# Performance work log

Hardware: AMD Instinct MI355X
Metric: run time of the kernel (lower is better)

## Reference

```python
import jax, jax.numpy as jnp
import numpy as np

D_H = 768
HEAD = 12
D_ATTN = D_H // HEAD


def setup_inputs() -> dict:
    key = jax.random.key(0)
    ks = jax.random.split(key, 9)
    bz, slen = 2, 4096
    scale = 1.0 / np.sqrt(D_H)
    return {
        "v": jax.random.normal(ks[0], (bz, slen, D_H), jnp.float32),
        "k": jax.random.normal(ks[1], (bz, slen, D_H), jnp.float32),
        "q": jax.random.normal(ks[2], (bz, slen, D_H), jnp.float32),
        "mask": jax.random.randint(ks[3], (bz, 1, 1, slen), 0, 2, jnp.int32),
        "w_v": jax.random.normal(ks[4], (D_H, D_H), jnp.float32) * scale,
        "w_k": jax.random.normal(ks[5], (D_H, D_H), jnp.float32) * scale,
        "w_q": jax.random.normal(ks[6], (D_H, D_H), jnp.float32) * scale,
        "w_o": jax.random.normal(ks[7], (D_H, D_H), jnp.float32) * scale,
        "b_o": jax.random.normal(ks[8], (D_H,), jnp.float32) * 0.02,
    }


def _split_head(x, seq_len):
    # (bz, len, d_h) -> (bz, head, len, d_attn)
    bz = x.shape[0]
    return x.reshape(bz, seq_len, HEAD, D_ATTN).transpose(0, 2, 1, 3)


def reference(v, k, q, mask, w_v, w_k, w_q, w_o, b_o):
    len_k, len_q = k.shape[1], q.shape[1]
    vh = _split_head(v @ w_v, len_k)   # (bz, head, len_k, d_attn)
    kh = _split_head(k @ w_k, len_k)
    qh = _split_head(q @ w_q, len_q)
    # scaled dot-product attention with additive mask
    weight = jnp.einsum("bhqd,bhkd->bhqk", qh, kh) / jnp.sqrt(
        jnp.asarray(D_ATTN, jnp.float32)
    )
    weight = weight + mask.astype(weight.dtype) * (-1e9)
    scale_weight = jax.nn.softmax(weight, axis=-1)
    attn = jnp.einsum("bhqk,bhkd->bhqd", scale_weight, vh)
    attn = attn.transpose(0, 2, 1, 3).reshape(-1, len_q, D_H)
    return attn @ w_o + b_o
```

## Files before the change

### kernel.cpp

```cpp
#include <hip/hip_runtime.h>
#include <hip/hip_bf16.h>

#define SLEN 4096
#define DH 768
#define NHEAD 12
#define DA 64

using short8 = __attribute__((ext_vector_type(8))) short;
using f32x4  = __attribute__((ext_vector_type(4))) float;
typedef unsigned uv2 __attribute__((ext_vector_type(2)));

static __device__ __forceinline__ unsigned short f2b(float f) {
    union { __hip_bfloat16 h; unsigned short u; } c;
    c.h = __float2bfloat16(f);
    return c.u;
}

static __device__ __forceinline__ unsigned pkbf(float a, float b) {
    __hip_bfloat162 h = __float22bfloat162_rn(float2{a, b});
    union { __hip_bfloat162 h; unsigned u; } c; c.h = h; return c.u;
}

static __device__ __forceinline__ float fexp2(float x) {
    float r; asm("v_exp_f32 %0, %1" : "=v"(r) : "v"(x)); return r;
}

static __device__ __forceinline__ void swap32(unsigned& a, unsigned& b, int g1) {
#if __has_builtin(__builtin_amdgcn_permlane32_swap)
    uv2 r = __builtin_amdgcn_permlane32_swap(a, b, false, false);
    a = r.x; b = r.y;
#else
    unsigned own = g1 ? b : a, send = g1 ? a : b;
    unsigned recv = __shfl_xor(send, 32);
    unsigned nlo = g1 ? recv : own;
    unsigned nhi = g1 ? own : recv;
    a = nlo; b = nhi;
#endif
}

static __device__ __forceinline__ void swap16(unsigned& a, unsigned& b, int g0) {
#if __has_builtin(__builtin_amdgcn_permlane16_swap)
    uv2 r = __builtin_amdgcn_permlane16_swap(a, b, false, false);
    a = r.x; b = r.y;
#else
    unsigned own = g0 ? b : a, send = g0 ? a : b;
    unsigned recv = __shfl_xor(send, 16);
    unsigned nlo = g0 ? recv : own;
    unsigned nhi = g0 ? own : recv;
    a = nlo; b = nhi;
#endif
}

#define GLD_LDS16(gp, lp) __builtin_amdgcn_global_load_lds( \
    (const __attribute__((address_space(1))) unsigned int*)(gp), \
    (__attribute__((address_space(3))) unsigned int*)(lp), 16, 0, 0)

#define CSCALE 0.18033688011f
#define BIASSTRIDE 4352

__global__ __launch_bounds__(256) void wtrans4(const float* __restrict__ w_v, const float* __restrict__ w_k,
                                               const float* __restrict__ w_q, const float* __restrict__ w_o,
                                               unsigned short* __restrict__ WtV, unsigned short* __restrict__ WtK,
                                               unsigned short* __restrict__ WtQ, unsigned short* __restrict__ WtO,
                                               const int* __restrict__ mask, int* __restrict__ idx,
                                               float* __restrict__ biasC, int* __restrict__ nktArr) {
    const int z = blockIdx.y;
    const int t = threadIdx.x;
    if (z == 4) {
        if (blockIdx.x >= 2) return;
        __shared__ int psum[256];
        const int b = blockIdx.x;
        const int s0 = t * 16;
        const int* mb = mask + b * SLEN;
        int keep[16]; int cnt = 0;
#pragma unroll
        for (int j = 0; j < 16; ++j) { keep[j] = (mb[s0 + j] == 0); cnt += keep[j]; }
        psum[t] = cnt;
        __syncthreads();
        for (int off = 1; off < 256; off <<= 1) {
            int v = psum[t];
            int u = (t >= off) ? psum[t - off] : 0;
            __syncthreads();
            psum[t] = v + u;
            __syncthreads();
        }
        int excl = psum[t] - cnt;
        int total = psum[255];
        int* ib = idx + b * SLEN;
#pragma unroll
        for (int j = 0; j < 16; ++j)
            if (keep[j]) ib[excl++] = s0 + j;
        for (int j = total + t; j < SLEN; j += 256) ib[j] = 0;
        int nkt = (total + 63) >> 6;
        if (nkt < 2) nkt = 2;
        if (t == 0) nktArr[b] = nkt;
        float* bb = biasC + b * BIASSTRIDE;
        for (int j = t; j < BIASSTRIDE; j += 256) bb[j] = (j < total) ? 0.f : -1.442695041e9f;
        return;
    }
    const float* W = (z == 0) ? w_v : (z == 1) ? w_k : (z == 2) ? w_q : w_o;
    unsigned short* Wt = (z == 0) ? WtV : (z == 1) ? WtK : (z == 2) ? WtQ : WtO;
    __shared__ float tile[64][65];
    const int tk = blockIdx.x / 12, tn = blockIdx.x % 12;
    const int k0 = tk * 64, n0 = tn * 64;
#pragma unroll
    for (int i = 0; i < 4; ++i) {
        int uid = t + 256 * i;
        int r = uid >> 4, c = (uid & 15) * 4;
        float4 v4 = *reinterpret_cast<const float4*>(W + (size_t)(k0 + r) * DH + n0 + c);
        tile[r][c] = v4.x; tile[r][c + 1] = v4.y; tile[r][c + 2] = v4.z; tile[r][c + 3] = v4.w;
    }
    __syncthreads();
#pragma unroll
    for (int i = 0; i < 2; ++i) {
        int uid = t + 256 * i;
        int n = uid >> 3, c = (uid & 7) * 8;
        union { unsigned short us[8]; uint4 u; } pk;
#pragma unroll
        for (int j = 0; j < 8; ++j) pk.us[j] = f2b(tile[c + j][n]);
        *reinterpret_cast<uint4*>(Wt + (size_t)(n0 + n) * DH + k0 + c) = pk.u;
    }
}

__global__ __launch_bounds__(256, 3) void proj3(const float* __restrict__ vin, const float* __restrict__ kin,
                                                const float* __restrict__ qin,
                                                const unsigned short* __restrict__ WtV,
                                                const unsigned short* __restrict__ WtK,
                                                const unsigned short* __restrict__ WtQ,
                                                unsigned short* __restrict__ Vh,
                                                unsigned short* __restrict__ Kh,
                                                unsigned short* __restrict__ Qh) {
    __shared__ __align__(16) char smem[49152];
    const int t = threadIdx.x;
    const int w = t >> 6, lane = t & 63, lr = lane & 15, lg = lane >> 4;
    const int zz = blockIdx.y;
    const int z = zz / 6, panel = zz % 6;
    const float* X = (z == 0) ? vin : (z == 1) ? kin : qin;
    const unsigned short* Wt = (z == 0) ? WtV : (z == 1) ? WtK : WtQ;
    const int row0 = blockIdx.x * 128;
    const int n0 = panel * 128;

    const float* ap[4];
#pragma unroll
    for (int g = 0; g < 4; ++g) {
        int row = w * 32 + g * 8 + (lane >> 3);
        int cj = (lane & 7) ^ (row & 7);
        ap[g] = X + (size_t)(row0 + row) * DH + cj * 4;
    }
    const unsigned short* bp2[2];
#pragma unroll
    for (int g = 0; g < 2; ++g) {
        int n = w * 32 + g * 16 + (lane >> 2);
        int cj = (lane & 3) ^ (n & 3);
        bp2[g] = Wt + (size_t)(n0 + n) * DH + cj * 8;
    }

    const int arow = w * 32 + lr;
    const int lr7 = lr & 7, lr3 = lr & 3;

    f32x4 acc[2][8] = {};

#define STAGE(PAR) do {                                                              \
        char* ab_ = smem + (PAR) * 16384 + w * 4096;                                 \
        char* bb_ = smem + 32768 + (PAR) * 8192 + w * 2048;                          \
        GLD_LDS16(ap[0], ab_);         GLD_LDS16(ap[1], ab_ + 1024);                 \
        GLD_LDS16(ap[2], ab_ + 2048);  GLD_LDS16(ap[3], ab_ + 3072);                 \
        GLD_LDS16(bp2[0], bb_);        GLD_LDS16(bp2[1], bb_ + 1024);                \
        ap[0] += 32; ap[1] += 32; ap[2] += 32; ap[3] += 32;                          \
        bp2[0] += 32; bp2[1] += 32;                                                  \
    } while (0)

    STAGE(0);
    __syncthreads();

    for (int kt = 0; kt < 24; ++kt) {
        const int par = kt & 1;
        if (kt < 23) STAGE(par ^ 1);
        const char* bufA = smem + par * 16384;
        const char* bufB = smem + 32768 + par * 8192;
        short8 af[2];
#pragma unroll
        for (int mi = 0; mi < 2; ++mi) {
            int r = arow + mi * 16;
            f32x4 alo = *reinterpret_cast<const f32x4*>(bufA + r * 128 + ((2 * lg) ^ lr7) * 16);
            f32x4 ahi = *reinterpret_cast<const f32x4*>(bufA + r * 128 + ((2 * lg + 1) ^ lr7) * 16);
            union { unsigned u[4]; short8 s; } pk;
            pk.u[0] = pkbf(alo[0], alo[1]);
            pk.u[1] = pkbf(alo[2], alo[3]);
            pk.u[2] = pkbf(ahi[0], ahi[1]);
            pk.u[3] = pkbf(ahi[2], ahi[3]);
            af[mi] = pk.s;
        }
        __builtin_amdgcn_s_setprio(1);
#pragma unroll
        for (int ni = 0; ni < 8; ++ni) {
            int n = ni * 16 + lr;
            short8 bf = *reinterpret_cast<const short8*>(bufB + n * 64 + (lg ^ lr3) * 16);
            acc[0][ni] = __builtin_amdgcn_mfma_f32_16x16x32_bf16(af[0], bf, acc[0][ni], 0, 0, 0);
            acc[1][ni] = __builtin_amdgcn_mfma_f32_16x16x32_bf16(af[1], bf, acc[1][ni], 0, 0, 0);
        }
        __builtin_amdgcn_s_setprio(0);
        __syncthreads();
    }
#undef STAGE

    const int b = row0 >> 12, s0 = row0 & 4095;
    unsigned short* Y = (z == 0) ? Vh : (z == 1) ? Kh : Qh;
    const float scale = (z == 2) ? CSCALE : 1.0f;
#pragma unroll
    for (int mi = 0; mi < 2; ++mi)
#pragma unroll
        for (int ni = 0; ni < 8; ++ni) {
            int n = n0 + ni * 16 + lr;
            int h = n >> 6, d = n & 63;
#pragma unroll
            for (int r = 0; r < 4; ++r) {
                int s = s0 + w * 32 + mi * 16 + lg * 4 + r;
                Y[(size_t)((b * NHEAD + h) * SLEN + s) * DA + d] = f2b(acc[mi][ni][r] * scale);
            }
        }
}

__global__ __launch_bounds__(256) void kvcompact(const unsigned short* __restrict__ Kh,
                                                 const unsigned short* __restrict__ Vh,
                                                 unsigned short* __restrict__ Khc,
                                                 unsigned short* __restrict__ VhTc,
                                                 const int* __restrict__ idx,
                                                 const int* __restrict__ nktArr) {
    const int jt = blockIdx.x;
    const int bh = blockIdx.y;
    const int b = bh / NHEAD;
    if (jt >= nktArr[b]) return;
    const int j0 = jt * 64;
    __shared__ unsigned short tile[64][72];
    const int t = threadIdx.x;
    const int r = t >> 2, c = t & 3;
    const int src = idx[b * SLEN + j0 + r];
    const size_t kin  = ((size_t)bh * SLEN + src) * DA + c * 16;
    const size_t kout = ((size_t)bh * SLEN + j0 + r) * DA + c * 16;
    uint4 kv0 = *reinterpret_cast<const uint4*>(Kh + kin);
    uint4 kv1 = *reinterpret_cast<const uint4*>(Kh + kin + 8);
    *reinterpret_cast<uint4*>(Khc + kout) = kv0;
    *reinterpret_cast<uint4*>(Khc + kout + 8) = kv1;
    uint4 vv0 = *reinterpret_cast<const uint4*>(Vh + kin);
    uint4 vv1 = *reinterpret_cast<const uint4*>(Vh + kin + 8);
    *reinterpret_cast<uint4*>(&tile[r][c * 16]) = vv0;
    *reinterpret_cast<uint4*>(&tile[r][c * 16 + 8]) = vv1;
    __syncthreads();
    const int d = t & 63, jc = (t >> 6) * 16;
    union { unsigned short us[8]; uint4 u; } p0, p1;
#pragma unroll
    for (int j = 0; j < 8; ++j) { p0.us[j] = tile[jc + j][d]; p1.us[j] = tile[jc + 8 + j][d]; }
    unsigned short* dst = VhTc + ((size_t)bh * DA + d) * SLEN + j0 + jc;
    *reinterpret_cast<uint4*>(dst) = p0.u;
    *reinterpret_cast<uint4*>(dst + 8) = p1.u;
}

__global__ __launch_bounds__(256, 3) void attn_kernel(const unsigned short* __restrict__ Qh,
                                                      const unsigned short* __restrict__ Kh,
                                                      const unsigned short* __restrict__ VhT,
                                                      const float* __restrict__ biasC,
                                                      const int* __restrict__ nktArr,
                                                      unsigned short* __restrict__ AT) {
    __shared__ __align__(16) char smem[49152];
    const int t = threadIdx.x;
    const int w = t >> 6, lane = t & 63, lr = lane & 15, lg = lane >> 4;
    const int g0 = (lane >> 4) & 1, g1 = (lane >> 5) & 1;
    const int lr7 = lr & 7;

    const int i = blockIdx.x;
    const int bh = (i & 7) * 3 + ((i >> 3) >> 5);
    const int qb = (i >> 3) & 31;
    const int b = bh / NHEAD;
    const int q0 = qb * 128;
    const size_t base = (size_t)bh * SLEN * DA;
    const int wq0 = q0 + w * 32;
    const int nkt = nktArr[b];

    short8 qf[2][2];
#pragma unroll
    for (int mi = 0; mi < 2; ++mi)
#pragma unroll
        for (int ks = 0; ks < 2; ++ks)
            qf[mi][ks] = *reinterpret_cast<const short8*>(
                Qh + base + (size_t)(wq0 + mi * 16 + lr) * DA + ks * 32 + lg * 8);

    const int uid0 = (w << 6) | lane;
    const int r0 = uid0 >> 3;
    const int sc0 = ((uid0 & 7) ^ (r0 & 7)) * 8;
    const unsigned short* kp = Kh + base + (size_t)r0 * DA + sc0;
    const unsigned short* vp = VhT + ((size_t)bh * DA + r0) * SLEN + sc0;
    const float* bp = biasC + b * BIASSTRIDE + lg * 4;

    const int a0 = lr * 128 + ((lg) ^ lr7) * 16;
    const int a1 = lr * 128 + ((4 + lg) ^ lr7) * 16;

    f32x4 st[2][4];
    f32x4 oacc[2][4] = {};
    f32x4 oacc_l[2] = {};
    f32x4 bias_c[4];
    short8 pa[2][2];
    union { unsigned u[4]; short8 s; } ones;
    ones.u[0] = 0x3F803F80u; ones.u[1] = 0x3F803F80u; ones.u[2] = 0x3F803F80u; ones.u[3] = 0x3F803F80u;

#define STAGE(CB) do {                                                   \
        GLD_LDS16(kp,              smem + (CB) + w * 1024);              \
        GLD_LDS16(kp + 2048,       smem + (CB) + (4 + w) * 1024);        \
        GLD_LDS16(vp,              smem + (CB) + 8192 + w * 1024);       \
        GLD_LDS16(vp + 32 * SLEN,  smem + (CB) + 8192 + (4 + w) * 1024); \
        kp += 64 * DA; vp += 64;                                         \
    } while (0)

#define BIASLD do {                                                              \
        _Pragma("unroll") for (int ni = 0; ni < 4; ++ni)                         \
            bias_c[ni] = *reinterpret_cast<const f32x4*>(bp + ni * 16);          \
        bp += 64;                                                                \
    } while (0)

#define QKT(NB) do {                                                                           \
        _Pragma("unroll") for (int ni = 0; ni < 4; ++ni) {                                     \
            short8 kf0 = *reinterpret_cast<const short8*>(smem + (NB) + ni * 2048 + a0);       \
            short8 kf1 = *reinterpret_cast<const short8*>(smem + (NB) + ni * 2048 + a1);       \
            st[0][ni] = __builtin_amdgcn_mfma_f32_16x16x32_bf16(kf1, qf[0][1],                 \
                        __builtin_amdgcn_mfma_f32_16x16x32_bf16(kf0, qf[0][0], bias_c[ni], 0, 0, 0), 0, 0, 0); \
            st[1][ni] = __builtin_amdgcn_mfma_f32_16x16x32_bf16(kf1, qf[1][1],                 \
                        __builtin_amdgcn_mfma_f32_16x16x32_bf16(kf0, qf[1][0], bias_c[ni], 0, 0, 0), 0, 0, 0); \
        }                                                                                      \
    } while (0)

#define PV(CB) do {                                                                                  \
        _Pragma("unroll") for (int ni = 0; ni < 4; ++ni) {                                           \
            short8 vf0 = *reinterpret_cast<const short8*>(smem + (CB) + 8192 + ni * 2048 + a0);      \
            short8 vf1 = *reinterpret_cast<const short8*>(smem + (CB) + 8192 + ni * 2048 + a1);      \
            oacc[0][ni] = __builtin_amdgcn_mfma_f32_16x16x32_bf16(vf0, pa[0][0], oacc[0][ni], 0, 0, 0); \
            oacc[0][ni] = __builtin_amdgcn_mfma_f32_16x16x32_bf16(vf1, pa[0][1], oacc[0][ni], 0, 0, 0); \
            oacc[1][ni] = __builtin_amdgcn_mfma_f32_16x16x32_bf16(vf0, pa[1][0], oacc[1][ni], 0, 0, 0); \
            oacc[1][ni] = __builtin_amdgcn_mfma_f32_16x16x32_bf16(vf1, pa[1][1], oacc[1][ni], 0, 0, 0); \
        }                                                                                            \
        oacc_l[0] = __builtin_amdgcn_mfma_f32_16x16x32_bf16(ones.s, pa[0][0], oacc_l[0], 0, 0, 0);   \
        oacc_l[0] = __builtin_amdgcn_mfma_f32_16x16x32_bf16(ones.s, pa[0][1], oacc_l[0], 0, 0, 0);   \
        oacc_l[1] = __builtin_amdgcn_mfma_f32_16x16x32_bf16(ones.s, pa[1][0], oacc_l[1], 0, 0, 0);   \
        oacc_l[1] = __builtin_amdgcn_mfma_f32_16x16x32_bf16(ones.s, pa[1][1], oacc_l[1], 0, 0, 0);   \
    } while (0)

#define SOFTMAX do {                                                                               \
        _Pragma("unroll") for (int mi = 0; mi < 2; ++mi) {                                         \
            unsigned D[8];                                                                         \
            _Pragma("unroll") for (int ni = 0; ni < 4; ++ni) {                                     \
                float p0 = fexp2(st[mi][ni][0]);                                                   \
                float p1 = fexp2(st[mi][ni][1]);                                                   \
                float p2 = fexp2(st[mi][ni][2]);                                                   \
                float p3 = fexp2(st[mi][ni][3]);                                                   \
                D[ni * 2] = pkbf(p0, p1);                                                          \
                D[ni * 2 + 1] = pkbf(p2, p3);                                                      \
            }                                                                                      \
            swap32(D[0], D[2], g1); swap32(D[1], D[3], g1);                                        \
            swap32(D[4], D[6], g1); swap32(D[5], D[7], g1);                                        \
            swap16(D[0], D[2], g0); swap16(D[1], D[3], g0);                                        \
            swap16(D[4], D[6], g0); swap16(D[4 - 4], D[2], g0);                                    \
            union { unsigned u[4]; short8 s; } c0, c1;                                             \
            c0.u[0] = D[0]; c0.u[1] = D[1]; c0.u[2] = D[2]; c0.u[3] = D[3];                        \
            c1.u[0] = D[4]; c1.u[1] = D[5]; c1.u[2] = D[6]; c1.u[3] = D[7];                        \
            pa[mi][0] = c0.s; pa[mi][1] = c1.s;                                                    \
        }                                                                                          \
    } while (0)

#undef SOFTMAX
#define SOFTMAX do {                                                                               \
        _Pragma("unroll") for (int mi = 0; mi < 2; ++mi) {                                         \
            unsigned D[8];                                                                         \
            _Pragma("unroll") for (int ni = 0; ni < 4; ++ni) {                                     \
                float p0 = fexp2(st[mi][ni][0]);                                                   \
                float p1 = fexp2(st[mi][ni][1]);                                                   \
                float p2 = fexp2(st[mi][ni][2]);                                                   \
                float p3 = fexp2(st[mi][ni][3]);                                                   \
                D[ni * 2] = pkbf(p0, p1);                                                          \
                D[ni * 2 + 1] = pkbf(p2, p3);                                                      \
            }                                                                                      \
            swap32(D[0], D[2], g1); swap32(D[1], D[3], g1);                                        \
            swap32(D[4], D[6], g1); swap32(D[5], D[7], g1);                                        \
            swap16(D[0], D[2], g0); swap16(D[1], D[3], g0);                                        \
            swap16(D[4], D[6], g0); swap16(D[5], D[7], g0);                                        \
            union { unsigned u[4]; short8 s; } c0, c1;                                             \
            c0.u[0] = D[0]; c0.u[1] = D[1]; c0.u[2] = D[2]; c0.u[3] = D[3];                        \
            c1.u[0] = D[4]; c1.u[1] = D[5]; c1.u[2] = D[6]; c1.u[3] = D[7];                        \
            pa[mi][0] = c0.s; pa[mi][1] = c1.s;                                                    \
        }                                                                                          \
    } while (0)

    STAGE(0);
    __syncthreads();
    STAGE(16384);
    BIASLD;
    __builtin_amdgcn_s_setprio(1);
    QKT(0);
    __builtin_amdgcn_s_setprio(0);

    int cb = 0, nb = 16384, nnb = 32768;
    for (int kt = 0; kt < nkt - 1; ++kt) {
        SOFTMAX;
        __syncthreads();
        if (kt < nkt - 2) STAGE(nnb);
        BIASLD;
        __builtin_amdgcn_s_setprio(1);
        QKT(nb);
        PV(cb);
        __builtin_amdgcn_s_setprio(0);
        int tmp = cb; cb = nb; nb = nnb; nnb = tmp;
    }
    SOFTMAX;
    __builtin_amdgcn_s_setprio(1);
    PV(cb);
    __builtin_amdgcn_s_setprio(0);

#undef SOFTMAX
#undef PV
#undef QKT
#undef BIASLD
#undef STAGE

    {
        __syncthreads();
        float inv[2];
        inv[0] = 1.0f / oacc_l[0][0];
        inv[1] = 1.0f / oacc_l[1][0];
        unsigned* Obw = reinterpret_cast<unsigned*>(smem) + w * (32 * 36);
#pragma unroll
        for (int mi = 0; mi < 2; ++mi)
#pragma unroll
            for (int ni = 0; ni < 4; ++ni) {
                uint2 pr;
                pr.x = pkbf(oacc[mi][ni][0] * inv[mi], oacc[mi][ni][1] * inv[mi]);
                pr.y = pkbf(oacc[mi][ni][2] * inv[mi], oacc[mi][ni][3] * inv[mi]);
                *reinterpret_cast<uint2*>(&Obw[(mi * 16 + lr) * 36 + ni * 8 + lg * 2]) = pr;
            }
        __syncthreads();
        int row = lane >> 1, half = lane & 1;
        int qg = q0 + w * 32 + row;
        unsigned short* dst = AT + (size_t)(b * SLEN + qg) * DH + (bh % NHEAD) * DA + half * 32;
#pragma unroll
        for (int c = 0; c < 4; ++c) {
            uint4 v = *reinterpret_cast<const uint4*>(&Obw[row * 36 + half * 16 + c * 4]);
            *reinterpret_cast<uint4*>(dst + c * 8) = v;
        }
    }
}

__global__ __launch_bounds__(256, 3) void proj_out(const unsigned short* __restrict__ X,
                                                   const unsigned short* __restrict__ Wt,
                                                   const float* __restrict__ bias,
                                                   float* __restrict__ Y) {
    __shared__ __align__(16) char smem[49152];
    const int t = threadIdx.x;
    const int w = t >> 6, lane = t & 63, lr = lane & 15, lg = lane >> 4;
    const int row0 = blockIdx.x * 128;
    const int n0 = blockIdx.y * 64;
    const int lr7 = lr & 7;

    const unsigned short* ap[4];
#pragma unroll
    for (int g = 0; g < 4; ++g) {
        int row = w * 32 + g * 8 + (lane >> 3);
        int cj = (lane & 7) ^ (row & 7);
        ap[g] = X + (size_t)(row0 + row) * DH + cj * 8;
    }
    const unsigned short* bp2[2];
#pragma unroll
    for (int g = 0; g < 2; ++g) {
        int n = w * 16 + g * 8 + (lane >> 3);
        int cj = (lane & 7) ^ (n & 7);
        bp2[g] = Wt + (size_t)(n0 + n) * DH + cj * 8;
    }

    f32x4 acc[2][4] = {};

#define STAGE_O(PAR) do {                                                            \
        char* ab_ = smem + (PAR) * 16384 + w * 4096;                                 \
        char* bb_ = smem + 32768 + (PAR) * 8192 + w * 2048;                          \
        GLD_LDS16(ap[0], ab_);         GLD_LDS16(ap[1], ab_ + 1024);                 \
        GLD_LDS16(ap[2], ab_ + 2048);  GLD_LDS16(ap[3], ab_ + 3072);                 \
        GLD_LDS16(bp2[0], bb_);        GLD_LDS16(bp2[1], bb_ + 1024);                \
        ap[0] += 64; ap[1] += 64; ap[2] += 64; ap[3] += 64;                          \
        bp2[0] += 64; bp2[1] += 64;                                                  \
    } while (0)

    STAGE_O(0);
    __syncthreads();

    for (int kt = 0; kt < 12; ++kt) {
        const int par = kt & 1;
        if (kt < 11) STAGE_O(par ^ 1);
        const char* bufA = smem + par * 16384;
        const char* bufB = smem + 32768 + par * 8192;
        short8 af[2][2], bf[4][2];
#pragma unroll
        for (int mi = 0; mi < 2; ++mi) {
            int r = w * 32 + mi * 16 + lr;
#pragma unroll
            for (int ks = 0; ks < 2; ++ks)
                af[mi][ks] = *reinterpret_cast<const short8*>(bufA + r * 128 + ((ks * 4 + lg) ^ lr7) * 16);
        }
#pragma unroll
        for (int ni = 0; ni < 4; ++ni) {
            int n = ni * 16 + lr;
#pragma unroll
            for (int ks = 0; ks < 2; ++ks)
                bf[ni][ks] = *reinterpret_cast<const short8*>(bufB + n * 128 + ((ks * 4 + lg) ^ lr7) * 16);
        }
        __builtin_amdgcn_s_setprio(1);
#pragma unroll
        for (int mi = 0; mi < 2; ++mi)
#pragma unroll
            for (int ni = 0; ni < 4; ++ni) {
                acc[mi][ni] = __builtin_amdgcn_mfma_f32_16x16x32_bf16(af[mi][0], bf[ni][0], acc[mi][ni], 0, 0, 0);
                acc[mi][ni] = __builtin_amdgcn_mfma_f32_16x16x32_bf16(af[mi][1], bf[ni][1], acc[mi][ni], 0, 0, 0);
            }
        __builtin_amdgcn_s_setprio(0);
        __syncthreads();
    }
#undef STAGE_O

#pragma unroll
    for (int ni = 0; ni < 4; ++ni) {
        float bv = bias[n0 + ni * 16 + lr];
#pragma unroll
        for (int mi = 0; mi < 2; ++mi)
#pragma unroll
            for (int r = 0; r < 4; ++r) {
                int row = row0 + w * 32 + mi * 16 + lg * 4 + r;
                Y[(size_t)row * DH + n0 + ni * 16 + lr] = acc[mi][ni][r] + bv;
            }
    }
}

extern "C" void kernel_launch(void* const* d_in, const int* in_sizes, int n_in,
                              void* d_out, int out_size, void* d_ws, size_t ws_size,
                              hipStream_t stream) {
    const float* v   = (const float*)d_in[0];
    const float* k   = (const float*)d_in[1];
    const float* q   = (const float*)d_in[2];
    const int*  mask = (const int*)d_in[3];
    const float* w_v = (const float*)d_in[4];
    const float* w_k = (const float*)d_in[5];
    const float* w_q = (const float*)d_in[6];
    const float* w_o = (const float*)d_in[7];
    const float* b_o = (const float*)d_in[8];
    float* out = (float*)d_out;

    char* ws = (char*)d_ws;
    unsigned short* Qh  = (unsigned short*)(ws);
    unsigned short* KhD = (unsigned short*)(ws + 12582912);
    unsigned short* VhD = (unsigned short*)(ws + 25165824);
    unsigned short* Khc = (unsigned short*)(ws + 37748736);
    unsigned short* VhTc= (unsigned short*)(ws + 50331648);
    unsigned short* AT  = KhD;
    unsigned short* WtV = (unsigned short*)(ws + 62914560);
    unsigned short* WtK = WtV + 589824;
    unsigned short* WtQ = WtK + 589824;
    unsigned short* WtO = WtQ + 589824;
    float* biasC = (float*)(ws + 67633152);
    int*   idxA  = (int*)(ws + 67667968);
    int*   nktA  = (int*)(ws + 67700736);

    wtrans4<<<dim3(144, 5), 256, 0, stream>>>(w_v, w_k, w_q, w_o, WtV, WtK, WtQ, WtO,
                                              mask, idxA, biasC, nktA);
    proj3<<<dim3(64, 18), 256, 0, stream>>>(v, k, q, WtV, WtK, WtQ, VhD, KhD, Qh);
    kvcompact<<<dim3(64, 24), 256, 0, stream>>>(KhD, VhD, Khc, VhTc, idxA, nktA);
    attn_kernel<<<768, 256, 0, stream>>>(Qh, Khc, VhTc, biasC, nktA, AT);
    proj_out<<<dim3(64, 12), 256, 0, stream>>>(AT, WtO, b_o, out);
}
```

Baseline: 147.0 us.

## Load V fragments directly from global memory into registers, halving LDS staging

V tiles are no longer staged through LDS. Each lane now loads its V^T MFMA fragments straight from global memory into registers just before the PV step, and only K is triple-buffered in shared memory, so LDS use drops from 48KB to 24KB. This removes the LDS traffic for V and may allow more resident blocks per CU. In exchange, V loads are no longer prefetched a stage ahead, so their global latency sits right before PV and may stall it. Register pressure also rises under the 3-waves launch bound. A dead duplicate softmax macro is also deleted.

```diff
diff --git a/kernel.cpp b/kernel.cpp
--- a/kernel.cpp
+++ b/kernel.cpp
@@ -262,7 +262,7 @@
                                                       const float* __restrict__ biasC,
                                                       const int* __restrict__ nktArr,
                                                       unsigned short* __restrict__ AT) {
-    __shared__ __align__(16) char smem[49152];
+    __shared__ __align__(16) char smem[24576];
     const int t = threadIdx.x;
     const int w = t >> 6, lane = t & 63, lr = lane & 15, lg = lane >> 4;
     const int g0 = (lane >> 4) & 1, g1 = (lane >> 5) & 1;
@@ -289,8 +289,11 @@
     const int r0 = uid0 >> 3;
     const int sc0 = ((uid0 & 7) ^ (r0 & 7)) * 8;
     const unsigned short* kp = Kh + base + (size_t)r0 * DA + sc0;
-    const unsigned short* vp = VhT + ((size_t)bh * DA + r0) * SLEN + sc0;
     const float* bp = biasC + b * BIASSTRIDE + lg * 4;
+    const unsigned short* vq[4];
+#pragma unroll
+    for (int ni = 0; ni < 4; ++ni)
+        vq[ni] = VhT + ((size_t)bh * DA + ni * 16 + lr) * SLEN + lg * 8;
 
     const int a0 = lr * 128 + ((lg) ^ lr7) * 16;
     const int a1 = lr * 128 + ((4 + lg) ^ lr7) * 16;
@@ -300,21 +303,28 @@
     f32x4 oacc_l[2] = {};
     f32x4 bias_c[4];
     short8 pa[2][2];
+    short8 vf[4][2];
     union { unsigned u[4]; short8 s; } ones;
     ones.u[0] = 0x3F803F80u; ones.u[1] = 0x3F803F80u; ones.u[2] = 0x3F803F80u; ones.u[3] = 0x3F803F80u;
 
 #define STAGE(CB) do {                                                   \
-        GLD_LDS16(kp,              smem + (CB) + w * 1024);              \
-        GLD_LDS16(kp + 2048,       smem + (CB) + (4 + w) * 1024);        \
-        GLD_LDS16(vp,              smem + (CB) + 8192 + w * 1024);       \
-        GLD_LDS16(vp + 32 * SLEN,  smem + (CB) + 8192 + (4 + w) * 1024); \
-        kp += 64 * DA; vp += 64;                                         \
+        GLD_LDS16(kp,        smem + (CB) + w * 1024);                    \
+        GLD_LDS16(kp + 2048, smem + (CB) + (4 + w) * 1024);              \
+        kp += 64 * DA;                                                   \
     } while (0)
 
 #define BIASLD do {                                                              \
         _Pragma("unroll") for (int ni = 0; ni < 4; ++ni)                         \
             bias_c[ni] = *reinterpret_cast<const f32x4*>(bp + ni * 16);          \
         bp += 64;                                                                \
+    } while (0)
+
+#define VFLOAD do {                                                              \
+        _Pragma("unroll") for (int ni = 0; ni < 4; ++ni) {                       \
+            vf[ni][0] = *reinterpret_cast<const short8*>(vq[ni]);                \
+            vf[ni][1] = *reinterpret_cast<const short8*>(vq[ni] + 32);           \
+            vq[ni] += 64;                                                        \
+        }                                                                        \
     } while (0)
 
 #define QKT(NB) do {                                                                           \
@@ -328,14 +338,12 @@
         }                                                                                      \
     } while (0)
 
-#define PV(CB) do {                                                                                  \
+#define PV do {                                                                                      \
         _Pragma("unroll") for (int ni = 0; ni < 4; ++ni) {                                           \
-            short8 vf0 = *reinterpret_cast<const short8*>(smem + (CB) + 8192 + ni * 2048 + a0);      \
-            short8 vf1 = *reinterpret_cast<const short8*>(smem + (CB) + 8192 + ni * 2048 + a1);      \
-            oacc[0][ni] = __builtin_amdgcn_mfma_f32_16x16x32_bf16(vf0, pa[0][0], oacc[0][ni], 0, 0, 0); \
-            oacc[0][ni] = __builtin_amdgcn_mfma_f32_16x16x32_bf16(vf1, pa[0][1], oacc[0][ni], 0, 0, 0); \
-            oacc[1][ni] = __builtin_amdgcn_mfma_f32_16x16x32_bf16(vf0, pa[1][0], oacc[1][ni], 0, 0, 0); \
-            oacc[1][ni] = __builtin_amdgcn_mfma_f32_16x16x32_bf16(vf1, pa[1][1], oacc[1][ni], 0, 0, 0); \
+            oacc[0][ni] = __builtin_amdgcn_mfma_f32_16x16x32_bf16(vf[ni][0], pa[0][0], oacc[0][ni], 0, 0, 0); \
+            oacc[0][ni] = __builtin_amdgcn_mfma_f32_16x16x32_bf16(vf[ni][1], pa[0][1], oacc[0][ni], 0, 0, 0); \
+            oacc[1][ni] = __builtin_amdgcn_mfma_f32_16x16x32_bf16(vf[ni][0], pa[1][0], oacc[1][ni], 0, 0, 0); \
+            oacc[1][ni] = __builtin_amdgcn_mfma_f32_16x16x32_bf16(vf[ni][1], pa[1][1], oacc[1][ni], 0, 0, 0); \
         }                                                                                            \
         oacc_l[0] = __builtin_amdgcn_mfma_f32_16x16x32_bf16(ones.s, pa[0][0], oacc_l[0], 0, 0, 0);   \
         oacc_l[0] = __builtin_amdgcn_mfma_f32_16x16x32_bf16(ones.s, pa[0][1], oacc_l[0], 0, 0, 0);   \
@@ -343,29 +351,6 @@
         oacc_l[1] = __builtin_amdgcn_mfma_f32_16x16x32_bf16(ones.s, pa[1][1], oacc_l[1], 0, 0, 0);   \
     } while (0)
 
-#define SOFTMAX do {                                                                               \
-        _Pragma("unroll") for (int mi = 0; mi < 2; ++mi) {                                         \
-            unsigned D[8];                                                                         \
-            _Pragma("unroll") for (int ni = 0; ni < 4; ++ni) {                                     \
-                float p0 = fexp2(st[mi][ni][0]);                                                   \
-                float p1 = fexp2(st[mi][ni][1]);                                                   \
-                float p2 = fexp2(st[mi][ni][2]);                                                   \
-                float p3 = fexp2(st[mi][ni][3]);                                                   \
-                D[ni * 2] = pkbf(p0, p1);                                                          \
-                D[ni * 2 + 1] = pkbf(p2, p3);                                                      \
-            }                                                                                      \
-            swap32(D[0], D[2], g1); swap32(D[1], D[3], g1);                                        \
-            swap32(D[4], D[6], g1); swap32(D[5], D[7], g1);                                        \
-            swap16(D[0], D[2], g0); swap16(D[1], D[3], g0);                                        \
-            swap16(D[4], D[6], g0); swap16(D[4 - 4], D[2], g0);                                    \
-            union { unsigned u[4]; short8 s; } c0, c1;                                             \
-            c0.u[0] = D[0]; c0.u[1] = D[1]; c0.u[2] = D[2]; c0.u[3] = D[3];                        \
-            c1.u[0] = D[4]; c1.u[1] = D[5]; c1.u[2] = D[6]; c1.u[3] = D[7];                        \
-            pa[mi][0] = c0.s; pa[mi][1] = c1.s;                                                    \
-        }                                                                                          \
-    } while (0)
-
-#undef SOFTMAX
 #define SOFTMAX do {                                                                               \
         _Pragma("unroll") for (int mi = 0; mi < 2; ++mi) {                                         \
             unsigned D[8];                                                                         \
@@ -390,32 +375,35 @@
 
     STAGE(0);
     __syncthreads();
-    STAGE(16384);
+    STAGE(8192);
     BIASLD;
     __builtin_amdgcn_s_setprio(1);
     QKT(0);
     __builtin_amdgcn_s_setprio(0);
 
-    int cb = 0, nb = 16384, nnb = 32768;
+    int cb = 0, nb = 8192, nnb = 16384;
     for (int kt = 0; kt < nkt - 1; ++kt) {
         SOFTMAX;
         __syncthreads();
         if (kt < nkt - 2) STAGE(nnb);
         BIASLD;
+        VFLOAD;
         __builtin_amdgcn_s_setprio(1);
         QKT(nb);
-        PV(cb);
+        PV;
         __builtin_amdgcn_s_setprio(0);
         int tmp = cb; cb = nb; nb = nnb; nnb = tmp;
     }
     SOFTMAX;
+    VFLOAD;
     __builtin_amdgcn_s_setprio(1);
-    PV(cb);
+    PV;
     __builtin_amdgcn_s_setprio(0);
 
 #undef SOFTMAX
 #undef PV
 #undef QKT
+#undef VFLOAD
 #undef BIASLD
 #undef STAGE
 
```

Result: slower. 199.9 us (+36.0%).

## Fuse KV compaction into projection kernel via gathered rows and transposed V store

Applied to the files above, without the earlier changes.

The projection kernel now gathers only the unmasked key/value rows through the compaction index and skips row blocks past the compacted length. K is written directly in compacted form, and V is transposed through shared memory and stored as VhT. This removes the separate kvcompact kernel, its intermediate full-size K/V buffers, and the projection work on masked rows. The cost is indirect row loads in the GEMM A path and an extra LDS transpose epilogue for V.

```diff
diff --git a/kernel.cpp b/kernel.cpp
--- a/kernel.cpp
+++ b/kernel.cpp
@@ -127,9 +127,11 @@
                                                 const unsigned short* __restrict__ WtV,
                                                 const unsigned short* __restrict__ WtK,
                                                 const unsigned short* __restrict__ WtQ,
-                                                unsigned short* __restrict__ Vh,
-                                                unsigned short* __restrict__ Kh,
-                                                unsigned short* __restrict__ Qh) {
+                                                unsigned short* __restrict__ VhTc,
+                                                unsigned short* __restrict__ Khc,
+                                                unsigned short* __restrict__ Qh,
+                                                const int* __restrict__ idx,
+                                                const int* __restrict__ nktArr) {
     __shared__ __align__(16) char smem[49152];
     const int t = threadIdx.x;
     const int w = t >> 6, lane = t & 63, lr = lane & 15, lg = lane >> 4;
@@ -137,15 +139,19 @@
     const int z = zz / 6, panel = zz % 6;
     const float* X = (z == 0) ? vin : (z == 1) ? kin : qin;
     const unsigned short* Wt = (z == 0) ? WtV : (z == 1) ? WtK : WtQ;
-    const int row0 = blockIdx.x * 128;
+    const int b = blockIdx.x >> 5;
+    const int r128 = (blockIdx.x & 31) * 128;
+    const bool gather = (z != 2);
+    if (gather && r128 >= nktArr[b] * 64) return;
     const int n0 = panel * 128;
 
     const float* ap[4];
 #pragma unroll
     for (int g = 0; g < 4; ++g) {
         int row = w * 32 + g * 8 + (lane >> 3);
+        int grow = b * SLEN + (gather ? idx[b * SLEN + r128 + row] : (r128 + row));
         int cj = (lane & 7) ^ (row & 7);
-        ap[g] = X + (size_t)(row0 + row) * DH + cj * 4;
+        ap[g] = X + (size_t)grow * DH + cj * 4;
     }
     const unsigned short* bp2[2];
 #pragma unroll
@@ -204,56 +210,40 @@
     }
 #undef STAGE
 
-    const int b = row0 >> 12, s0 = row0 & 4095;
-    unsigned short* Y = (z == 0) ? Vh : (z == 1) ? Kh : Qh;
-    const float scale = (z == 2) ? CSCALE : 1.0f;
-#pragma unroll
-    for (int mi = 0; mi < 2; ++mi)
-#pragma unroll
-        for (int ni = 0; ni < 8; ++ni) {
-            int n = n0 + ni * 16 + lr;
-            int h = n >> 6, d = n & 63;
-#pragma unroll
-            for (int r = 0; r < 4; ++r) {
-                int s = s0 + w * 32 + mi * 16 + lg * 4 + r;
-                Y[(size_t)((b * NHEAD + h) * SLEN + s) * DA + d] = f2b(acc[mi][ni][r] * scale);
+    if (z == 0) {
+        unsigned short (*tile)[136] = reinterpret_cast<unsigned short(*)[136]>(smem);
+#pragma unroll
+        for (int mi = 0; mi < 2; ++mi)
+#pragma unroll
+            for (int ni = 0; ni < 8; ++ni) {
+                int n = ni * 16 + lr;
+                int j = w * 32 + mi * 16 + lg * 4;
+                *reinterpret_cast<unsigned*>(&tile[n][j])     = pkbf(acc[mi][ni][0], acc[mi][ni][1]);
+                *reinterpret_cast<unsigned*>(&tile[n][j + 2]) = pkbf(acc[mi][ni][2], acc[mi][ni][3]);
             }
-        }
-}
-
-__global__ __launch_bounds__(256) void kvcompact(const unsigned short* __restrict__ Kh,
-                                                 const unsigned short* __restrict__ Vh,
-                                                 unsigned short* __restrict__ Khc,
-                                                 unsigned short* __restrict__ VhTc,
-                                                 const int* __restrict__ idx,
-                                                 const int* __restrict__ nktArr) {
-    const int jt = blockIdx.x;
-    const int bh = blockIdx.y;
-    const int b = bh / NHEAD;
-    if (jt >= nktArr[b]) return;
-    const int j0 = jt * 64;
-    __shared__ unsigned short tile[64][72];
-    const int t = threadIdx.x;
-    const int r = t >> 2, c = t & 3;
-    const int src = idx[b * SLEN + j0 + r];
-    const size_t kin  = ((size_t)bh * SLEN + src) * DA + c * 16;
-    const size_t kout = ((size_t)bh * SLEN + j0 + r) * DA + c * 16;
-    uint4 kv0 = *reinterpret_cast<const uint4*>(Kh + kin);
-    uint4 kv1 = *reinterpret_cast<const uint4*>(Kh + kin + 8);
-    *reinterpret_cast<uint4*>(Khc + kout) = kv0;
-    *reinterpret_cast<uint4*>(Khc + kout + 8) = kv1;
-    uint4 vv0 = *reinterpret_cast<const uint4*>(Vh + kin);
-    uint4 vv1 = *reinterpret_cast<const uint4*>(Vh + kin + 8);
-    *reinterpret_cast<uint4*>(&tile[r][c * 16]) = vv0;
-    *reinterpret_cast<uint4*>(&tile[r][c * 16 + 8]) = vv1;
-    __syncthreads();
-    const int d = t & 63, jc = (t >> 6) * 16;
-    union { unsigned short us[8]; uint4 u; } p0, p1;
-#pragma unroll
-    for (int j = 0; j < 8; ++j) { p0.us[j] = tile[jc + j][d]; p1.us[j] = tile[jc + 8 + j][d]; }
-    unsigned short* dst = VhTc + ((size_t)bh * DA + d) * SLEN + j0 + jc;
-    *reinterpret_cast<uint4*>(dst) = p0.u;
-    *reinterpret_cast<uint4*>(dst + 8) = p1.u;
+        __syncthreads();
+        int n = t >> 1, jc = (t & 1) * 64;
+        unsigned short* dst = VhTc +
+            ((size_t)(b * NHEAD + 2 * panel + (n >> 6)) * DA + (n & 63)) * SLEN + r128 + jc;
+#pragma unroll
+        for (int c = 0; c < 8; ++c)
+            *reinterpret_cast<uint4*>(dst + c * 8) = *reinterpret_cast<const uint4*>(&tile[n][jc + c * 8]);
+    } else {
+        unsigned short* Y = (z == 1) ? Khc : Qh;
+        const float scale = (z == 2) ? CSCALE : 1.0f;
+#pragma unroll
+        for (int mi = 0; mi < 2; ++mi)
+#pragma unroll
+            for (int ni = 0; ni < 8; ++ni) {
+                int n = n0 + ni * 16 + lr;
+                int h = n >> 6, d = n & 63;
+#pragma unroll
+                for (int r = 0; r < 4; ++r) {
+                    int s = r128 + w * 32 + mi * 16 + lg * 4 + r;
+                    Y[(size_t)((b * NHEAD + h) * SLEN + s) * DA + d] = f2b(acc[mi][ni][r] * scale);
+                }
+            }
+    }
 }
 
 __global__ __launch_bounds__(256, 3) void attn_kernel(const unsigned short* __restrict__ Qh,
@@ -343,29 +333,6 @@
         oacc_l[1] = __builtin_amdgcn_mfma_f32_16x16x32_bf16(ones.s, pa[1][1], oacc_l[1], 0, 0, 0);   \
     } while (0)
 
-#define SOFTMAX do {                                                                               \
-        _Pragma("unroll") for (int mi = 0; mi < 2; ++mi) {                                         \
-            unsigned D[8];                                                                         \
-            _Pragma("unroll") for (int ni = 0; ni < 4; ++ni) {                                     \
-                float p0 = fexp2(st[mi][ni][0]);                                                   \
-                float p1 = fexp2(st[mi][ni][1]);                                                   \
-                float p2 = fexp2(st[mi][ni][2]);                                                   \
-                float p3 = fexp2(st[mi][ni][3]);                                                   \
-                D[ni * 2] = pkbf(p0, p1);                                                          \
-                D[ni * 2 + 1] = pkbf(p2, p3);                                                      \
-            }                                                                                      \
-            swap32(D[0], D[2], g1); swap32(D[1], D[3], g1);                                        \
-            swap32(D[4], D[6], g1); swap32(D[5], D[7], g1);                                        \
-            swap16(D[0], D[2], g0); swap16(D[1], D[3], g0);                                        \
-            swap16(D[4], D[6], g0); swap16(D[4 - 4], D[2], g0);                                    \
-            union { unsigned u[4]; short8 s; } c0, c1;                                             \
-            c0.u[0] = D[0]; c0.u[1] = D[1]; c0.u[2] = D[2]; c0.u[3] = D[3];                        \
-            c1.u[0] = D[4]; c1.u[1] = D[5]; c1.u[2] = D[6]; c1.u[3] = D[7];                        \
-            pa[mi][0] = c0.s; pa[mi][1] = c1.s;                                                    \
-        }                                                                                          \
-    } while (0)
-
-#undef SOFTMAX
 #define SOFTMAX do {                                                                               \
         _Pragma("unroll") for (int mi = 0; mi < 2; ++mi) {                                         \
             unsigned D[8];                                                                         \
@@ -548,24 +515,21 @@
     float* out = (float*)d_out;
 
     char* ws = (char*)d_ws;
-    unsigned short* Qh  = (unsigned short*)(ws);
-    unsigned short* KhD = (unsigned short*)(ws + 12582912);
-    unsigned short* VhD = (unsigned short*)(ws + 25165824);
-    unsigned short* Khc = (unsigned short*)(ws + 37748736);
-    unsigned short* VhTc= (unsigned short*)(ws + 50331648);
-    unsigned short* AT  = KhD;
-    unsigned short* WtV = (unsigned short*)(ws + 62914560);
-    unsigned short* WtK = WtV + 589824;
-    unsigned short* WtQ = WtK + 589824;
-    unsigned short* WtO = WtQ + 589824;
-    float* biasC = (float*)(ws + 67633152);
-    int*   idxA  = (int*)(ws + 67667968);
-    int*   nktA  = (int*)(ws + 67700736);
+    unsigned short* Qh   = (unsigned short*)(ws);
+    unsigned short* Khc  = (unsigned short*)(ws + 12582912);
+    unsigned short* AT   = (unsigned short*)(ws + 25165824);
+    unsigned short* VhTc = (unsigned short*)(ws + 37748736);
+    unsigned short* WtV  = (unsigned short*)(ws + 50331648);
+    unsigned short* WtK  = WtV + 589824;
+    unsigned short* WtQ  = WtK + 589824;
+    unsigned short* WtO  = WtQ + 589824;
+    float* biasC = (float*)(ws + 55050240);
+    int*   idxA  = (int*)(ws + 55085056);
+    int*   nktA  = (int*)(ws + 55117824);
 
     wtrans4<<<dim3(144, 5), 256, 0, stream>>>(w_v, w_k, w_q, w_o, WtV, WtK, WtQ, WtO,
                                               mask, idxA, biasC, nktA);
-    proj3<<<dim3(64, 18), 256, 0, stream>>>(v, k, q, WtV, WtK, WtQ, VhD, KhD, Qh);
-    kvcompact<<<dim3(64, 24), 256, 0, stream>>>(KhD, VhD, Khc, VhTc, idxA, nktA);
+    proj3<<<dim3(64, 18), 256, 0, stream>>>(v, k, q, WtV, WtK, WtQ, VhTc, Khc, Qh, idxA, nktA);
     attn_kernel<<<768, 256, 0, stream>>>(Qh, Khc, VhTc, biasC, nktA, AT);
     proj_out<<<dim3(64, 12), 256, 0, stream>>>(AT, WtO, b_o, out);
 }
```

Measured after the change: 137.7 us. 1.07x faster.
